# Kernel optimization log

Measured on AMD Instinct MI355X. Metric: run time of the kernel, lower is better.

The kernel has to match this reference:

```python
import jax, jax.numpy as jnp
import numpy as np

B, T, C, H = 8, 2048, 1024, 64  # batch, context_length, embedding_dim, head_size


def setup_inputs() -> dict:
    key = jax.random.key(0)
    kx, kq, kk, kv = jax.random.split(key, 4)
    s = C ** -0.5  # linear-init-like scale
    return {
        "x": jax.random.normal(kx, (B, T, C), dtype=jnp.float32),
        "Wq": jax.random.normal(kq, (C, H), dtype=jnp.float32) * s,
        "Wk": jax.random.normal(kk, (C, H), dtype=jnp.float32) * s,
        "Wv": jax.random.normal(kv, (C, H), dtype=jnp.float32) * s,
    }


def reference(x, Wq, Wk, Wv):
    Bx, Tx, _ = x.shape
    q = jnp.einsum('btc,ch->bth', x, Wq)
    k = jnp.einsum('btc,ch->bth', x, Wk)
    v = jnp.einsum('btc,ch->bth', x, Wv)
    scale = k.shape[-1] ** -0.5
    scores = jnp.einsum('bth,bsh->bts', q, k) * scale  # [B, T, T]
    causal = jnp.tril(jnp.ones((Tx, Tx), dtype=bool))
    scores = jnp.where(causal, scores, -jnp.inf)
    weights = jax.nn.softmax(scores, axis=-1)
    # dropout is identity in eval mode
    out = jnp.einsum('bts,bsh->bth', weights, v)  # [B, T, H]
    return out
```

## Files before the change

### kernel.cpp

```cpp
#include <hip/hip_runtime.h>
#include <hip/hip_bf16.h>

#define BB 8
#define TT 2048
#define CC 1024
#define HH 64

typedef float f32x4 __attribute__((ext_vector_type(4)));
typedef float f32x16 __attribute__((ext_vector_type(16)));
typedef short s16x8 __attribute__((ext_vector_type(8)));

static __device__ __forceinline__ unsigned short f2bf(float f) {
    unsigned int u = __float_as_uint(f);
    u = (u + 0x7FFFu + ((u >> 16) & 1u)) >> 16;
    return (unsigned short)u;
}

static __device__ __forceinline__ unsigned cvt_pk_bf16(float lo, float hi) {
    unsigned r;
    asm("v_cvt_pk_bf16_f32 %0, %1, %2" : "=v"(r) : "v"(lo), "v"(hi));
    return r;
}

__global__ __launch_bounds__(256) void wt_kernel(
    const float* __restrict__ Wq, const float* __restrict__ Wk,
    const float* __restrict__ Wv, unsigned short* __restrict__ wTf) {
    const int e8 = blockIdx.x * 256 + threadIdx.x;
    const int lane = e8 & 63;
    const int s = (e8 >> 6) & 31;
    const int n16 = e8 >> 11;
    const int sel = n16 >> 2;
    const float* W = (sel == 0) ? Wq : ((sel == 1) ? Wk : Wv);
    const int h = ((n16 & 3) << 4) + (lane & 15);
    const int cb = s * 32 + ((lane >> 4) << 3);
    s16x8 v;
#pragma unroll
    for (int j = 0; j < 8; ++j) v[j] = (short)f2bf(W[(size_t)(cb + j) * HH + h]);
    *reinterpret_cast<s16x8*>(&wTf[(size_t)e8 * 8]) = v;
}

__global__ __launch_bounds__(512, 4) void qkv_kernel(
    const float* __restrict__ x, const unsigned short* __restrict__ wTf,
    unsigned short* __restrict__ Qf, unsigned short* __restrict__ Kf,
    unsigned short* __restrict__ Vf) {
    __shared__ unsigned short xb[2][32 * 256];
    const int tid = threadIdx.x;
    const int wv = tid >> 6, lane = tid & 63;
    const int lo = lane & 15, hi = lane >> 4;
    const int wm = wv >> 2, wn = wv & 3;
    const int rb = blockIdx.x * 32;
    const int b_ = rb >> 11, tile = (rb & (TT - 1)) >> 5;

    const int srow = tid >> 4, sc = (tid & 15) * 16;
    const float* xsrc = &x[(size_t)(rb + srow) * CC + sc];
    const int swz = (srow & 15) << 3;
    const int wg0 = srow * 256 + (sc ^ swz);
    const int wg1 = srow * 256 + ((sc + 8) ^ swz);

    const int arow = wm * 16 + lo;
    const int abase = arow * 256;
    const int aswz = (arow & 15) << 3;

    f32x4 acc[3];
#pragma unroll
    for (int n = 0; n < 3; ++n) acc[n] = (f32x4){0.f, 0.f, 0.f, 0.f};

    f32x4 pf[4];
#pragma unroll
    for (int i = 0; i < 4; ++i) pf[i] = *reinterpret_cast<const f32x4*>(xsrc + 4 * i);

    s16x8 bv[3][3];
#define BLOAD(SET, SLOT)                                                       \
    {                                                                          \
        _Pragma("unroll")                                                      \
        for (int n = 0; n < 3; ++n)                                            \
            bv[SET][n] = *reinterpret_cast<const s16x8*>(                      \
                &wTf[(((size_t)(wn * 3 + n) * 32 + (SLOT)) * 64 + lane) * 8]); \
    }
    BLOAD(0, 0)
    BLOAD(1, 1)

#pragma unroll
    for (int c = 0; c < 4; ++c) {
        unsigned short* wb = xb[c & 1];
        s16x8 w0, w1;
        w0[0] = (short)f2bf(pf[0][0]); w0[1] = (short)f2bf(pf[0][1]);
        w0[2] = (short)f2bf(pf[0][2]); w0[3] = (short)f2bf(pf[0][3]);
        w0[4] = (short)f2bf(pf[1][0]); w0[5] = (short)f2bf(pf[1][1]);
        w0[6] = (short)f2bf(pf[1][2]); w0[7] = (short)f2bf(pf[1][3]);
        w1[0] = (short)f2bf(pf[2][0]); w1[1] = (short)f2bf(pf[2][1]);
        w1[2] = (short)f2bf(pf[2][2]); w1[3] = (short)f2bf(pf[2][3]);
        w1[4] = (short)f2bf(pf[3][0]); w1[5] = (short)f2bf(pf[3][1]);
        w1[6] = (short)f2bf(pf[3][2]); w1[7] = (short)f2bf(pf[3][3]);
        *reinterpret_cast<s16x8*>(&wb[wg0]) = w0;
        *reinterpret_cast<s16x8*>(&wb[wg1]) = w1;
        __syncthreads();
        if (c < 3) {
#pragma unroll
            for (int i = 0; i < 4; ++i)
                pf[i] = *reinterpret_cast<const f32x4*>(xsrc + (c + 1) * 256 + 4 * i);
        }
        const unsigned short* base = xb[c & 1];
#pragma unroll
        for (int kh = 0; kh < 8; ++kh) {
            const int slot = c * 8 + kh;
            if (slot + 2 < 32) BLOAD((slot + 2) % 3, slot + 2)
            const s16x8 a = *reinterpret_cast<const s16x8*>(
                &base[abase + ((kh * 32 + hi * 8) ^ aswz)]);
#pragma unroll
            for (int n = 0; n < 3; ++n)
                acc[n] = __builtin_amdgcn_mfma_f32_16x16x32_bf16(a, bv[slot % 3][n], acc[n], 0, 0, 0);
        }
    }
#undef BLOAD

    __syncthreads();
    unsigned short* fr = reinterpret_cast<unsigned short*>(xb);
#pragma unroll
    for (int n = 0; n < 3; ++n) {
        const int n16 = wn * 3 + n;
        const int sel = n16 >> 2;
#pragma unroll
        for (int r = 0; r < 4; ++r) {
            const int tok31 = wm * 16 + 4 * hi + r;
            const unsigned short bvv = f2bf(acc[n][r]);
            if (sel == 0) {
                const int s = n16, half = (lo >> 3) & 1, j = lo & 7;
                fr[(s * 64 + half * 32 + tok31) * 8 + j] = bvv;
            } else if (sel == 1) {
                const int s = n16 - 4, half = (lo >> 3) & 1, j = lo & 7;
                fr[2048 + (s * 64 + half * 32 + tok31) * 8 + j] = bvv;
            } else {
                const int h = (n16 - 8) * 16 + lo;
                const int mt = h >> 5;
                const int s2 = tok31 >> 4, hf = (tok31 >> 3) & 1, jj = tok31 & 7;
                fr[4096 + ((mt * 2 + s2) * 64 + hf * 32 + (h & 31)) * 8 + jj] = bvv;
            }
        }
    }
    __syncthreads();
    const size_t tb = ((size_t)b_ * 64 + tile) * 2048;
    if (tid < 256) {
        *reinterpret_cast<s16x8*>(&Qf[tb + tid * 8]) =
            *reinterpret_cast<const s16x8*>(&fr[tid * 8]);
    } else {
        *reinterpret_cast<s16x8*>(&Kf[tb + (tid - 256) * 8]) =
            *reinterpret_cast<const s16x8*>(&fr[2048 + (tid - 256) * 8]);
    }
    if (tid < 256) {
        *reinterpret_cast<s16x8*>(&Vf[tb + tid * 8]) =
            *reinterpret_cast<const s16x8*>(&fr[4096 + tid * 8]);
    }
}

__global__ __launch_bounds__(512, 4) void attn_kernel(
    const unsigned short* __restrict__ Qf, const unsigned short* __restrict__ Kf,
    const unsigned short* __restrict__ Vf, float* __restrict__ out) {
    __shared__ __align__(16) char smem[33792 + 2048];
    float (*OfL)[64][33] = reinterpret_cast<float(*)[64][33]>(smem);
    float (*Mm)[32] = reinterpret_cast<float(*)[32]>(smem + 33792);
    float (*Ml)[32] = reinterpret_cast<float(*)[32]>(smem + 33792 + 1024);

    const int tid = threadIdx.x;
    const int wv = tid >> 6, lane = tid & 63;
    const int q = lane & 31, half = lane >> 5;
    const int b = blockIdx.x & 7;
    const int qt = 63 - (blockIdx.x >> 3);
    const int qbase = qt * 32;
    const float CEXP = 0.125f * 1.44269504f;

    const unsigned short* qp = &Qf[(((size_t)b * 64 + qt) * 256 + lane) * 8];
    s16x8 qf[4];
#pragma unroll
    for (int s = 0; s < 4; ++s) qf[s] = *reinterpret_cast<const s16x8*>(qp + s * 512);

    f32x16 oA, oB;
#pragma unroll
    for (int r = 0; r < 16; ++r) { oA[r] = 0.f; oB[r] = 0.f; }
    float m = -1e30f, l = 0.f;

    for (int t = wv; t <= qt; t += 8) {
        const unsigned short* vp = &Vf[(((size_t)b * 64 + t) * 256 + lane) * 8];
        s16x8 vf[4];
#pragma unroll
        for (int i = 0; i < 4; ++i)
            vf[i] = *reinterpret_cast<const s16x8*>(vp + i * 512);
        const unsigned short* kp = &Kf[(((size_t)b * 64 + t) * 256 + lane) * 8];
        f32x16 sa;
#pragma unroll
        for (int r = 0; r < 16; ++r) sa[r] = 0.f;
#pragma unroll
        for (int s = 0; s < 4; ++s) {
            const s16x8 kf = *reinterpret_cast<const s16x8*>(kp + s * 512);
            sa = __builtin_amdgcn_mfma_f32_32x32x16_bf16(kf, qf[s], sa, 0, 0, 0);
        }
        if (t == qt) {
#pragma unroll
            for (int r = 0; r < 16; ++r) {
                const int key = 4 * half + (r & 3) + 8 * (r >> 2);
                if (key > q) sa[r] = -1e30f;
            }
        }
        float pmax = sa[0];
#pragma unroll
        for (int r = 1; r < 16; ++r) pmax = fmaxf(pmax, sa[r]);
        pmax = fmaxf(pmax, __shfl_xor(pmax, 32));
        if (!__all(pmax <= m + 64.f)) {
            const float mnew = fmaxf(m, pmax);
            const float alpha = exp2f((m - mnew) * CEXP);
            l *= alpha;
#pragma unroll
            for (int r = 0; r < 16; ++r) { oA[r] *= alpha; oB[r] *= alpha; }
            m = mnew;
        }
        float rs = 0.f;
#pragma unroll
        for (int r = 0; r < 16; ++r) {
            const float p = exp2f((sa[r] - m) * CEXP);
            sa[r] = p;
            rs += p;
        }
        l += rs + __shfl_xor(rs, 32);
        unsigned d[8];
#pragma unroll
        for (int i = 0; i < 8; ++i) d[i] = cvt_pk_bf16(sa[2 * i], sa[2 * i + 1]);
        const unsigned snd0 = half ? d[0] : d[2];
        const unsigned snd1 = half ? d[1] : d[3];
        const unsigned snd2 = half ? d[4] : d[6];
        const unsigned snd3 = half ? d[5] : d[7];
        const unsigned rcv0 = __shfl_xor(snd0, 32);
        const unsigned rcv1 = __shfl_xor(snd1, 32);
        const unsigned rcv2 = __shfl_xor(snd2, 32);
        const unsigned rcv3 = __shfl_xor(snd3, 32);
        union { unsigned u[4]; s16x8 v; } f0, f1;
        f0.u[0] = half ? rcv0 : d[0];
        f0.u[1] = half ? rcv1 : d[1];
        f0.u[2] = half ? d[2] : rcv0;
        f0.u[3] = half ? d[3] : rcv1;
        f1.u[0] = half ? rcv2 : d[4];
        f1.u[1] = half ? rcv3 : d[5];
        f1.u[2] = half ? d[6] : rcv2;
        f1.u[3] = half ? d[7] : rcv3;
        oA = __builtin_amdgcn_mfma_f32_32x32x16_bf16(vf[0], f0.v, oA, 0, 0, 0);
        oB = __builtin_amdgcn_mfma_f32_32x32x16_bf16(vf[2], f0.v, oB, 0, 0, 0);
        oA = __builtin_amdgcn_mfma_f32_32x32x16_bf16(vf[1], f1.v, oA, 0, 0, 0);
        oB = __builtin_amdgcn_mfma_f32_32x32x16_bf16(vf[3], f1.v, oB, 0, 0, 0);
    }

#define PUBLISH(slot)                                                      \
    {                                                                      \
        _Pragma("unroll")                                                  \
        for (int r = 0; r < 16; ++r) {                                     \
            const int h0 = (r & 3) + 8 * (r >> 2) + 4 * half;              \
            OfL[slot][h0][q] = oA[r];                                      \
            OfL[slot][h0 + 32][q] = oB[r];                                 \
        }                                                                  \
    }
#define MERGE(slot, srcw)                                                  \
    {                                                                      \
        const float mb = Mm[srcw][q], lb = Ml[srcw][q];                    \
        const float M = fmaxf(m, mb);                                      \
        const float wa = exp2f((m - M) * CEXP);                            \
        const float wb = exp2f((mb - M) * CEXP);                           \
        _Pragma("unroll")                                                  \
        for (int r = 0; r < 16; ++r) {                                     \
            const int h0 = (r & 3) + 8 * (r >> 2) + 4 * half;              \
            oA[r] = oA[r] * wa + OfL[slot][h0][q] * wb;                    \
            oB[r] = oB[r] * wa + OfL[slot][h0 + 32][q] * wb;               \
        }                                                                  \
        l = l * wa + lb * wb;                                              \
        m = M;                                                             \
    }

    if (lane < 32) { Mm[wv][q] = m; Ml[wv][q] = l; }
    if (wv >= 4) PUBLISH(wv - 4);
    __syncthreads();
    if (wv < 4) MERGE(wv, wv + 4);
    __syncthreads();
    if (wv == 2 || wv == 3) {
        PUBLISH(wv - 2);
        if (lane < 32) { Mm[wv][q] = m; Ml[wv][q] = l; }
    }
    __syncthreads();
    if (wv < 2) MERGE(wv, wv + 2);
    __syncthreads();
    if (wv == 1) {
        PUBLISH(1);
        if (lane < 32) { Mm[1][q] = m; Ml[1][q] = l; }
    }
    __syncthreads();
    if (wv == 0) {
        MERGE(1, 1);
        const float inv = 1.f / l;
#pragma unroll
        for (int r = 0; r < 16; ++r) {
            const int h0 = (r & 3) + 8 * (r >> 2) + 4 * half;
            OfL[0][h0][q] = oA[r] * inv;
            OfL[0][h0 + 32][q] = oB[r] * inv;
        }
    }
    __syncthreads();
#pragma unroll
    for (int i = 0; i < 4; ++i) {
        const int idx = tid + 512 * i;
        const int h = idx & 63, q2 = idx >> 6;
        out[((size_t)b * TT + qbase + q2) * HH + h] = OfL[0][h][q2];
    }
#undef PUBLISH
#undef MERGE
}

extern "C" void kernel_launch(void* const* d_in, const int* in_sizes, int n_in,
                              void* d_out, int out_size, void* d_ws, size_t ws_size,
                              hipStream_t stream) {
    (void)in_sizes; (void)n_in; (void)out_size; (void)ws_size;
    const float* x  = (const float*)d_in[0];
    const float* Wq = (const float*)d_in[1];
    const float* Wk = (const float*)d_in[2];
    const float* Wv = (const float*)d_in[3];
    float* out = (float*)d_out;

    char* ws = (char*)d_ws;
    unsigned short* wTf = (unsigned short*)ws;
    unsigned short* Qf  = (unsigned short*)(ws + 393216);
    unsigned short* Kf  = (unsigned short*)(ws + 393216 + 2097152);
    unsigned short* Vf  = (unsigned short*)(ws + 393216 + 4194304);

    wt_kernel<<<96, 256, 0, stream>>>(Wq, Wk, Wv, wTf);
    qkv_kernel<<<512, 512, 0, stream>>>(x, wTf, Qf, Kf, Vf);
    attn_kernel<<<512, 512, 0, stream>>>(Qf, Kf, Vf, out);
}
```

Baseline: 52.84 us.

## Halve QKV projection tile to 16 rows with 256-thread blocks

The QKV projection kernel now processes 16 token rows per block with 4 waves instead of 32 rows with 8 waves, and launches twice as many blocks. The x staging buffer shrinks to 128-column chunks with an 8-step double-buffered pipeline, and the epilogue scatters half-tiles into the packed Q/K/V fragment layouts using a row-half index. The aim is more blocks for better occupancy and load balance across CUs. The cost is that each Wq/Wk/Wv fragment is reloaded by twice as many blocks, and there are more barriers per block.

Result: faster. 47.44 us (-10.2%).

```diff
diff --git a/kernel.cpp b/kernel.cpp
--- a/kernel.cpp
+++ b/kernel.cpp
@@ -39,35 +39,33 @@
     *reinterpret_cast<s16x8*>(&wTf[(size_t)e8 * 8]) = v;
 }
 
-__global__ __launch_bounds__(512, 4) void qkv_kernel(
+__global__ __launch_bounds__(256, 4) void qkv_kernel(
     const float* __restrict__ x, const unsigned short* __restrict__ wTf,
     unsigned short* __restrict__ Qf, unsigned short* __restrict__ Kf,
     unsigned short* __restrict__ Vf) {
-    __shared__ unsigned short xb[2][32 * 256];
+    __shared__ unsigned short xb[2][16 * 128];
     const int tid = threadIdx.x;
-    const int wv = tid >> 6, lane = tid & 63;
+    const int wn = tid >> 6, lane = tid & 63;
     const int lo = lane & 15, hi = lane >> 4;
-    const int wm = wv >> 2, wn = wv & 3;
-    const int rb = blockIdx.x * 32;
-    const int b_ = rb >> 11, tile = (rb & (TT - 1)) >> 5;
-
-    const int srow = tid >> 4, sc = (tid & 15) * 16;
-    const float* xsrc = &x[(size_t)(rb + srow) * CC + sc];
-    const int swz = (srow & 15) << 3;
-    const int wg0 = srow * 256 + (sc ^ swz);
-    const int wg1 = srow * 256 + ((sc + 8) ^ swz);
-
-    const int arow = wm * 16 + lo;
-    const int abase = arow * 256;
-    const int aswz = (arow & 15) << 3;
+    const int rb = blockIdx.x * 16;
+    const int mhat = (rb >> 4) & 1;
+
+    const int srow = tid >> 4, sc8 = (tid & 15) * 8;
+    const float* xsrc = &x[(size_t)(rb + srow) * CC + sc8];
+    const int swz = (srow & 7) << 3;
+    const int woff = srow * 128 + (sc8 ^ swz);
+
+    const int ab0 = lo * 128, as0 = (lo & 7) << 3;
 
     f32x4 acc[3];
 #pragma unroll
     for (int n = 0; n < 3; ++n) acc[n] = (f32x4){0.f, 0.f, 0.f, 0.f};
 
-    f32x4 pf[4];
-#pragma unroll
-    for (int i = 0; i < 4; ++i) pf[i] = *reinterpret_cast<const f32x4*>(xsrc + 4 * i);
+    f32x4 pfA[2], pfB[2];
+    pfA[0] = *reinterpret_cast<const f32x4*>(xsrc);
+    pfA[1] = *reinterpret_cast<const f32x4*>(xsrc + 4);
+    pfB[0] = *reinterpret_cast<const f32x4*>(xsrc + 128);
+    pfB[1] = *reinterpret_cast<const f32x4*>(xsrc + 128 + 4);
 
     s16x8 bv[3][3];
 #define BLOAD(SET, SLOT)                                                       \
@@ -81,32 +79,33 @@
     BLOAD(1, 1)
 
 #pragma unroll
-    for (int c = 0; c < 4; ++c) {
-        unsigned short* wb = xb[c & 1];
-        s16x8 w0, w1;
-        w0[0] = (short)f2bf(pf[0][0]); w0[1] = (short)f2bf(pf[0][1]);
-        w0[2] = (short)f2bf(pf[0][2]); w0[3] = (short)f2bf(pf[0][3]);
-        w0[4] = (short)f2bf(pf[1][0]); w0[5] = (short)f2bf(pf[1][1]);
-        w0[6] = (short)f2bf(pf[1][2]); w0[7] = (short)f2bf(pf[1][3]);
-        w1[0] = (short)f2bf(pf[2][0]); w1[1] = (short)f2bf(pf[2][1]);
-        w1[2] = (short)f2bf(pf[2][2]); w1[3] = (short)f2bf(pf[2][3]);
-        w1[4] = (short)f2bf(pf[3][0]); w1[5] = (short)f2bf(pf[3][1]);
-        w1[6] = (short)f2bf(pf[3][2]); w1[7] = (short)f2bf(pf[3][3]);
-        *reinterpret_cast<s16x8*>(&wb[wg0]) = w0;
-        *reinterpret_cast<s16x8*>(&wb[wg1]) = w1;
+    for (int c = 0; c < 8; ++c) {
+        {
+            const f32x4* pf = (c & 1) ? pfB : pfA;
+            s16x8 w;
+            w[0] = (short)f2bf(pf[0][0]); w[1] = (short)f2bf(pf[0][1]);
+            w[2] = (short)f2bf(pf[0][2]); w[3] = (short)f2bf(pf[0][3]);
+            w[4] = (short)f2bf(pf[1][0]); w[5] = (short)f2bf(pf[1][1]);
+            w[6] = (short)f2bf(pf[1][2]); w[7] = (short)f2bf(pf[1][3]);
+            *reinterpret_cast<s16x8*>(&xb[c & 1][woff]) = w;
+        }
         __syncthreads();
-        if (c < 3) {
-#pragma unroll
-            for (int i = 0; i < 4; ++i)
-                pf[i] = *reinterpret_cast<const f32x4*>(xsrc + (c + 1) * 256 + 4 * i);
+        if (c < 6) {
+            if (c & 1) {
+                pfB[0] = *reinterpret_cast<const f32x4*>(xsrc + (c + 2) * 128);
+                pfB[1] = *reinterpret_cast<const f32x4*>(xsrc + (c + 2) * 128 + 4);
+            } else {
+                pfA[0] = *reinterpret_cast<const f32x4*>(xsrc + (c + 2) * 128);
+                pfA[1] = *reinterpret_cast<const f32x4*>(xsrc + (c + 2) * 128 + 4);
+            }
         }
         const unsigned short* base = xb[c & 1];
 #pragma unroll
-        for (int kh = 0; kh < 8; ++kh) {
-            const int slot = c * 8 + kh;
+        for (int kh = 0; kh < 4; ++kh) {
+            const int slot = c * 4 + kh;
             if (slot + 2 < 32) BLOAD((slot + 2) % 3, slot + 2)
             const s16x8 a = *reinterpret_cast<const s16x8*>(
-                &base[abase + ((kh * 32 + hi * 8) ^ aswz)]);
+                &base[ab0 + ((kh * 32 + hi * 8) ^ as0)]);
 #pragma unroll
             for (int n = 0; n < 3; ++n)
                 acc[n] = __builtin_amdgcn_mfma_f32_16x16x32_bf16(a, bv[slot % 3][n], acc[n], 0, 0, 0);
@@ -122,34 +121,44 @@
         const int sel = n16 >> 2;
 #pragma unroll
         for (int r = 0; r < 4; ++r) {
-            const int tok31 = wm * 16 + 4 * hi + r;
+            const int tl = 4 * hi + r;
             const unsigned short bvv = f2bf(acc[n][r]);
             if (sel == 0) {
                 const int s = n16, half = (lo >> 3) & 1, j = lo & 7;
-                fr[(s * 64 + half * 32 + tok31) * 8 + j] = bvv;
+                fr[(s * 2 + half) * 128 + tl * 8 + j] = bvv;
             } else if (sel == 1) {
                 const int s = n16 - 4, half = (lo >> 3) & 1, j = lo & 7;
-                fr[2048 + (s * 64 + half * 32 + tok31) * 8 + j] = bvv;
+                fr[1024 + (s * 2 + half) * 128 + tl * 8 + j] = bvv;
             } else {
                 const int h = (n16 - 8) * 16 + lo;
-                const int mt = h >> 5;
-                const int s2 = tok31 >> 4, hf = (tok31 >> 3) & 1, jj = tok31 & 7;
-                fr[4096 + ((mt * 2 + s2) * 64 + hf * 32 + (h & 31)) * 8 + jj] = bvv;
+                const int mt = h >> 5, h31 = h & 31;
+                const int hf = tl >> 3, jj = tl & 7;
+                fr[2048 + (mt * 2 + hf) * 256 + h31 * 8 + jj] = bvv;
             }
         }
     }
     __syncthreads();
+    const int b_ = rb >> 11;
+    const int tile = (rb & (TT - 1)) >> 5;
     const size_t tb = ((size_t)b_ * 64 + tile) * 2048;
-    if (tid < 256) {
-        *reinterpret_cast<s16x8*>(&Qf[tb + tid * 8]) =
-            *reinterpret_cast<const s16x8*>(&fr[tid * 8]);
-    } else {
-        *reinterpret_cast<s16x8*>(&Kf[tb + (tid - 256) * 8]) =
-            *reinterpret_cast<const s16x8*>(&fr[2048 + (tid - 256) * 8]);
-    }
-    if (tid < 256) {
-        *reinterpret_cast<s16x8*>(&Vf[tb + tid * 8]) =
-            *reinterpret_cast<const s16x8*>(&fr[4096 + tid * 8]);
+#pragma unroll
+    for (int i = 0; i < 2; ++i) {
+        const int g = tid + 256 * i;
+        if (g < 384) {
+            const s16x8 val = *reinterpret_cast<const s16x8*>(&fr[g * 8]);
+            if (g < 256) {
+                const int u = g & 127;
+                const int s = u >> 5, half = (u >> 4) & 1, t = u & 15;
+                unsigned short* dst = (g < 128) ? Qf : Kf;
+                *reinterpret_cast<s16x8*>(
+                    &dst[tb + (size_t)(s * 64 + half * 32 + mhat * 16 + t) * 8]) = val;
+            } else {
+                const int u = g - 256;
+                const int mt = u >> 6, hf = (u >> 5) & 1, g32 = u & 31;
+                *reinterpret_cast<s16x8*>(
+                    &Vf[tb + (size_t)((mt * 2 + mhat) * 64 + hf * 32 + g32) * 8]) = val;
+            }
+        }
     }
 }
 
@@ -327,6 +336,6 @@
     unsigned short* Vf  = (unsigned short*)(ws + 393216 + 4194304);
 
     wt_kernel<<<96, 256, 0, stream>>>(Wq, Wk, Wv, wTf);
-    qkv_kernel<<<512, 512, 0, stream>>>(x, wTf, Qf, Kf, Vf);
+    qkv_kernel<<<1024, 256, 0, stream>>>(x, wTf, Qf, Kf, Vf);
     attn_kernel<<<512, 512, 0, stream>>>(Qf, Kf, Vf, out);
 }
```
